# Optimization experiments

Hardware: AMD Instinct MI355X
Metric: run time of the kernel (lower is better)

## Reference

```python
import jax, jax.numpy as jnp
import numpy as np

NUM_HEADS = 16

def setup_inputs() -> dict:
    key = jax.random.key(0)
    ks = jax.random.split(key, 5)
    b, c, w, h = 2, 1024, 48, 48
    sc = 0.02
    return {
        "x": jax.random.normal(ks[0], (b, c, w, h), jnp.float32),
        "Wqkv": jax.random.normal(ks[1], (3 * c, c), jnp.float32) * sc,
        "bqkv": jax.random.normal(ks[2], (3 * c,), jnp.float32) * sc,
        "Wo": jax.random.normal(ks[3], (c, c), jnp.float32) * sc,
        "bo": jax.random.normal(ks[4], (c,), jnp.float32) * sc,
    }

def reference(x, Wqkv, bqkv, Wo, bo):
    b, c, w, h = x.shape
    n = NUM_HEADS
    hd = c // n
    s = w * h
    # [b,c,w,h] -> tokens [b, s, c]
    xs = x.transpose(0, 2, 3, 1).reshape(b, s, c)
    qkv = xs @ Wqkv.T + bqkv                       # [b, s, 3c]
    # rearrange 'b s (three n hd) -> three b n s hd'
    qkv = qkv.reshape(b, s, 3, n, hd).transpose(2, 0, 3, 1, 4)
    q, k, v = qkv[0], qkv[1], qkv[2]               # [b, n, s, hd]
    score = jnp.einsum('bnqh,bnkh->bnqk', q, k) / jnp.sqrt(jnp.float32(hd))
    # module uses a soft causal mask: subtract 10000 above the diagonal
    mask = 10000.0 * jnp.triu(jnp.ones((s, s), dtype=score.dtype), k=1)
    attn = jax.nn.softmax(score - mask, axis=-1)   # [b, n, s, s]
    z = jnp.einsum('bnqk,bnkh->bqnh', attn, v).reshape(b, s, c)
    out = z @ Wo.T + bo                            # [b, s, c]
    return out.reshape(b, w, h, c).transpose(0, 3, 1, 2)
```

## Files before the change

kernel.cpp:

```cpp
#include <hip/hip_runtime.h>

typedef __bf16 bf16;
typedef __bf16 bf16x8 __attribute__((ext_vector_type(8)));
typedef float floatx4 __attribute__((ext_vector_type(4)));

static constexpr int S = 2304;
static constexpr int C = 1024;
static constexpr int NHEAD = 16;
static constexpr int HDIM = 64;
static constexpr int BATCH = 2;
static constexpr float QSCALE = 0.18033688011112042f;
static constexpr int QSPLIT = 12;
static constexpr int NACC = S - QSPLIT * 64;

__global__ __launch_bounds__(256) void k_zero(float4* __restrict__ p, int n4) {
  int i = blockIdx.x * 256 + threadIdx.x;
  if (i < n4) p[i] = float4{0.f, 0.f, 0.f, 0.f};
}

__global__ __launch_bounds__(256) void k_convert2(const float* __restrict__ s1,
                                                  bf16* __restrict__ d1, int n1,
                                                  const float* __restrict__ s2,
                                                  bf16* __restrict__ d2) {
  int i = blockIdx.x * 256 + threadIdx.x;
  const float* s;
  bf16* d;
  int idx;
  if (i < n1) { s = s1; d = d1; idx = i; }
  else        { s = s2; d = d2; idx = i - n1; }
  float4 a = *(const float4*)(s + (size_t)idx * 8);
  float4 b = *(const float4*)(s + (size_t)idx * 8 + 4);
  bf16x8 o;
  o[0] = (bf16)a.x; o[1] = (bf16)a.y; o[2] = (bf16)a.z; o[3] = (bf16)a.w;
  o[4] = (bf16)b.x; o[5] = (bf16)b.y; o[6] = (bf16)b.z; o[7] = (bf16)b.w;
  *(bf16x8*)(d + (size_t)idx * 8) = o;
}

__global__ __launch_bounds__(256) void k_transpose(const float* __restrict__ x,
                                                   bf16* __restrict__ xs) {
  __shared__ bf16 T[64 * 72];
  int c0 = blockIdx.x * 64, t0 = blockIdx.y * 64, b = blockIdx.z;
  int tid = threadIdx.x;
  const float* xb = x + (size_t)b * C * S;
#pragma unroll
  for (int it = 0; it < 4; ++it) {
    int idx = it * 256 + tid;
    int rc = idx >> 4, t4 = idx & 15;
    float4 v = *(const float4*)(xb + (size_t)(c0 + rc) * S + t0 + t4 * 4);
    T[(t4 * 4 + 0) * 72 + rc] = (bf16)v.x;
    T[(t4 * 4 + 1) * 72 + rc] = (bf16)v.y;
    T[(t4 * 4 + 2) * 72 + rc] = (bf16)v.z;
    T[(t4 * 4 + 3) * 72 + rc] = (bf16)v.w;
  }
  __syncthreads();
  bf16* xsb = xs + (size_t)b * S * C;
#pragma unroll
  for (int it = 0; it < 2; ++it) {
    int idx = it * 256 + tid;
    int rt = idx >> 3, c8 = idx & 7;
    bf16x8 v;
#pragma unroll
    for (int i = 0; i < 8; ++i) v[i] = T[rt * 72 + c8 * 8 + i];
    *(bf16x8*)(xsb + (size_t)(t0 + rt) * C + c0 + c8 * 8) = v;
  }
}

__device__ __forceinline__ void g2l16(const bf16* g, bf16* l) {
  __builtin_amdgcn_global_load_lds(
      (const __attribute__((address_space(1))) void*)g,
      (__attribute__((address_space(3))) void*)l, 16, 0, 0);
}

template <int EPI>
__global__ __launch_bounds__(256) void k_gemm_bt(const bf16* __restrict__ A,
                                                 const bf16* __restrict__ Bt,
                                                 const float* __restrict__ bias,
                                                 bf16* __restrict__ q,
                                                 bf16* __restrict__ k,
                                                 bf16* __restrict__ v,
                                                 float* __restrict__ outf) {
  constexpr int K = C;
  __shared__ bf16 As[128 * 64];
  __shared__ bf16 Bs[128 * 64];
  int tid = threadIdx.x;
  int w = tid >> 6, lane = tid & 63, ln = lane & 15, quad = lane >> 4;
  int m0 = blockIdx.y * 128, n0 = blockIdx.x * 128;
  int moff = (w >> 1) * 64, noff = (w & 1) * 64;
  floatx4 acc[4][4] = {};

  int sr[4], sc[4];
#pragma unroll
  for (int it = 0; it < 4; ++it) {
    int L = (it * 4 + w) * 64 + lane;
    sr[it] = L >> 3;
    sc[it] = (L & 7) ^ (sr[it] & 7);
  }

  for (int k0 = 0; k0 < K; k0 += 64) {
    __syncthreads();
#pragma unroll
    for (int it = 0; it < 4; ++it) {
      int cb = (it * 4 + w) * 64;
      g2l16(A + (size_t)(m0 + sr[it]) * K + k0 + sc[it] * 8, As + cb * 8);
      g2l16(Bt + (size_t)(n0 + sr[it]) * K + k0 + sc[it] * 8, Bs + cb * 8);
    }
    __syncthreads();
#pragma unroll
    for (int t = 0; t < 2; ++t) {
      bf16x8 af[4], bfr[4];
#pragma unroll
      for (int i = 0; i < 4; ++i) {
        int ra = moff + i * 16 + ln;
        af[i]  = *(const bf16x8*)(As + ra * 64 + (((t * 4 + quad) ^ (ra & 7))) * 8);
        int rb = noff + i * 16 + ln;
        bfr[i] = *(const bf16x8*)(Bs + rb * 64 + (((t * 4 + quad) ^ (rb & 7))) * 8);
      }
#pragma unroll
      for (int im = 0; im < 4; ++im)
#pragma unroll
        for (int in = 0; in < 4; ++in)
          acc[im][in] = __builtin_amdgcn_mfma_f32_16x16x32_bf16(
              af[im], bfr[in], acc[im][in], 0, 0, 0);
    }
  }

  int bidx = (m0 >= S) ? 1 : 0;
  if (EPI == 0) {
#pragma unroll
    for (int in = 0; in < 4; ++in) {
      int j = n0 + noff + in * 16 + ln;
      float bv = bias[j];
      int three = j >> 10;
      int head = (j >> 6) & 15;
      int hdi = j & 63;
#pragma unroll
      for (int im = 0; im < 4; ++im) {
        int mbase = m0 + moff + im * 16 + quad * 4;
        int tb = mbase - bidx * S;
        if (three == 2) {
          union { ushort4 u; bf16 h[4]; } P;
#pragma unroll
          for (int r = 0; r < 4; ++r) P.h[r] = (bf16)(acc[im][in][r] + bv);
          *(ushort4*)(v + ((size_t)(bidx * NHEAD + head) * HDIM + hdi) * S + tb) = P.u;
        } else if (three == 0) {
          bf16* dst = q + ((size_t)(bidx * NHEAD + head) * S + tb) * HDIM + hdi;
#pragma unroll
          for (int r = 0; r < 4; ++r)
            dst[(size_t)r * HDIM] = (bf16)((acc[im][in][r] + bv) * QSCALE);
        } else {
          bf16* dst = k + ((size_t)(bidx * NHEAD + head) * S + tb) * HDIM + hdi;
#pragma unroll
          for (int r = 0; r < 4; ++r) dst[(size_t)r * HDIM] = (bf16)(acc[im][in][r] + bv);
        }
      }
    }
  } else {
#pragma unroll
    for (int in = 0; in < 4; ++in) {
      int co = n0 + noff + in * 16 + ln;
      float bv = bias[co];
#pragma unroll
      for (int im = 0; im < 4; ++im) {
        int mbase = m0 + moff + im * 16 + quad * 4;
        int tb = mbase - bidx * S;
        float4 st;
        st.x = acc[im][in][0] + bv;
        st.y = acc[im][in][1] + bv;
        st.z = acc[im][in][2] + bv;
        st.w = acc[im][in][3] + bv;
        *(float4*)(outf + ((size_t)bidx * C + co) * S + tb) = st;
      }
    }
  }
}

__global__ __launch_bounds__(256) void k_attn_part(const bf16* __restrict__ Qg,
                                                   const bf16* __restrict__ Kg,
                                                   const bf16* __restrict__ Vtg,
                                                   bf16* __restrict__ z,
                                                   float* __restrict__ Oacc,
                                                   float* __restrict__ Lacc) {
  __shared__ bf16 Ks[2][64 * 64];
  __shared__ bf16 Vs[2][64 * 64];
  __shared__ bf16 Pt[64 * 64];
  int i = blockIdx.x;
  int xcd = i & 7, jj = i >> 3;
  int grp = jj / 72, j = jj % 72;
  int bh = xcd + 8 * grp;
  int qi, lo, hi;
  bool single = false;
  if (j < 36) {
    qi = 35 - j / 3;
    int c = j % 3;
    lo = c * (qi + 1) / 3;
    hi = (c + 1) * (qi + 1) / 3;
  } else if (j < 60) {
    int t = j - 36;
    qi = 23 - (t >> 1);
    int c = t & 1;
    lo = c * (qi + 1) / 2;
    hi = (c + 1) * (qi + 1) / 2;
  } else {
    qi = 71 - j;
    lo = 0;
    hi = qi + 1;
    single = true;
  }
  int b = bh >> 4, h = bh & 15;
  int tid = threadIdx.x;
  int w = tid >> 6, lane = tid & 63, ln = lane & 15, quad = lane >> 4;
  int q0 = qi * 64;
  int qg = q0 + w * 16 + ln;

  const bf16* kb = Kg + (size_t)bh * S * HDIM;
  const bf16* vb = Vtg + (size_t)bh * HDIM * S;

  int s_row = tid >> 3, s_c8 = tid & 7;
  int s_cs = s_c8 ^ (s_row & 7);
  int s_row2 = s_row + 32;
  int s_cs2 = s_c8 ^ (s_row2 & 7);
  size_t kOff1 = (size_t)s_row * HDIM + s_cs * 8;
  size_t kOff2 = (size_t)s_row2 * HDIM + s_cs2 * 8;
  size_t vOff1 = (size_t)s_row * S + s_cs * 8;
  size_t vOff2 = (size_t)s_row2 * S + s_cs2 * 8;

  const bf16* qb = Qg + ((size_t)bh * S + qg) * HDIM + quad * 8;
  bf16x8 qf0 = *(const bf16x8*)qb;
  bf16x8 qf1 = *(const bf16x8*)(qb + 32);

  float lsum = 0.f;
  floatx4 o_acc[4] = {};

  int prow = w * 16 + ln;
  int psw = ln & 7;
  bf16* ptw = Pt + prow * 64 + (quad & 1) * 4;
  const bf16* ptr = Pt + prow * 64;

  const bf16* kb0 = kb + (size_t)lo * 64 * HDIM;
  const bf16* vb0 = vb + (size_t)lo * 64;
  g2l16(kb0 + kOff1, Ks[0] + tid * 8);
  g2l16(vb0 + vOff1, Vs[0] + tid * 8);
  g2l16(kb0 + kOff2, Ks[0] + (256 + tid) * 8);
  g2l16(vb0 + vOff2, Vs[0] + (256 + tid) * 8);

  const bf16* kbn = kb0 + (size_t)64 * HDIM;
  const bf16* vbn = vb0 + 64;

#pragma unroll 1
  for (int kt = lo; kt < hi; ++kt) {
    int cur = (kt - lo) & 1;
    __syncthreads();

    if (kt + 1 < hi) {
      bf16* kd = Ks[1 - cur];
      bf16* vd = Vs[1 - cur];
      g2l16(kbn + kOff1, kd + tid * 8);
      g2l16(vbn + vOff1, vd + tid * 8);
      g2l16(kbn + kOff2, kd + (256 + tid) * 8);
      g2l16(vbn + vOff2, vd + (256 + tid) * 8);
      kbn += (size_t)64 * HDIM;
      vbn += 64;
    }

    floatx4 s_acc[4] = {};
#pragma unroll
    for (int kf = 0; kf < 4; ++kf) {
      int row = kf * 16 + ln;
      int sw = row & 7;
      bf16x8 k0 = *(const bf16x8*)(Ks[cur] + row * 64 + (sw ^ quad) * 8);
      bf16x8 k1 = *(const bf16x8*)(Ks[cur] + row * 64 + ((4 ^ sw) ^ quad) * 8);
      s_acc[kf] = __builtin_amdgcn_mfma_f32_16x16x32_bf16(k0, qf0, s_acc[kf], 0, 0, 0);
      s_acc[kf] = __builtin_amdgcn_mfma_f32_16x16x32_bf16(k1, qf1, s_acc[kf], 0, 0, 0);
    }

    if (kt < qi) {
#pragma unroll
      for (int kf = 0; kf < 4; ++kf) {
        union { ushort4 u; bf16 hh[4]; } P;
#pragma unroll
        for (int rr = 0; rr < 4; ++rr) {
          float pv = exp2f(s_acc[kf][rr]);
          lsum += pv;
          P.hh[rr] = (bf16)pv;
        }
        *(ushort4*)(ptw + (((kf * 2 + (quad >> 1)) ^ psw)) * 8) = P.u;
      }
    } else {
#pragma unroll
      for (int kf = 0; kf < 4; ++kf) {
        union { ushort4 u; bf16 hh[4]; } P;
#pragma unroll
        for (int rr = 0; rr < 4; ++rr) {
          int kl = kf * 16 + quad * 4 + rr;
          float pv = (kl > w * 16 + ln) ? 0.f : exp2f(s_acc[kf][rr]);
          lsum += pv;
          P.hh[rr] = (bf16)pv;
        }
        *(ushort4*)(ptw + (((kf * 2 + (quad >> 1)) ^ psw)) * 8) = P.u;
      }
    }

#pragma unroll
    for (int t = 0; t < 2; ++t) {
      bf16x8 pf = *(const bf16x8*)(ptr + (((t * 4 + quad) ^ psw)) * 8);
#pragma unroll
      for (int hf = 0; hf < 4; ++hf) {
        int row = hf * 16 + ln;
        int sw = row & 7;
        bf16x8 vf = *(const bf16x8*)(Vs[cur] + row * 64 + (((t * 4 + quad) ^ sw)) * 8);
        o_acc[hf] = __builtin_amdgcn_mfma_f32_16x16x32_bf16(vf, pf, o_acc[hf], 0, 0, 0);
      }
    }
  }

  lsum += __shfl_xor(lsum, 16);
  lsum += __shfl_xor(lsum, 32);

  if (single) {
    float inv = 1.f / lsum;
    bf16* dst = z + ((size_t)b * S + qg) * C + h * HDIM + quad * 4;
#pragma unroll
    for (int hf = 0; hf < 4; ++hf) {
      union { ushort4 u; bf16 hh[4]; } P;
#pragma unroll
      for (int rr = 0; rr < 4; ++rr) P.hh[rr] = (bf16)(o_acc[hf][rr] * inv);
      *(ushort4*)(dst + hf * 16) = P.u;
    }
  } else {
    int qa = qg - QSPLIT * 64;
    if (lane < 16) atomicAdd(&Lacc[bh * NACC + qa], lsum);
#pragma unroll
    for (int hf = 0; hf < 4; ++hf)
#pragma unroll
      for (int rr = 0; rr < 4; ++rr)
        atomicAdd(&Oacc[((size_t)bh * 64 + hf * 16 + quad * 4 + rr) * NACC + qa],
                  o_acc[hf][rr]);
  }
}

__global__ __launch_bounds__(256) void k_norm(const float* __restrict__ Oacc,
                                              const float* __restrict__ Lacc,
                                              bf16* __restrict__ z) {
  __shared__ float T[64 * 65];
  int qt = blockIdx.x, bh = blockIdx.y;
  int b = bh >> 4, h = bh & 15;
  int qrel0 = qt * 64;
  int q0 = QSPLIT * 64 + qrel0;
  int tid = threadIdx.x;
  int q4 = (tid & 15) * 4, hd0 = tid >> 4;
  float4 lv = *(const float4*)(Lacc + bh * NACC + qrel0 + q4);
  float inv0 = 1.f / lv.x, inv1 = 1.f / lv.y, inv2 = 1.f / lv.z, inv3 = 1.f / lv.w;
#pragma unroll
  for (int hf = 0; hf < 4; ++hf) {
    int hd = hf * 16 + hd0;
    float4 v = *(const float4*)(Oacc + ((size_t)bh * 64 + hd) * NACC + qrel0 + q4);
    T[(q4 + 0) * 65 + hd] = v.x * inv0;
    T[(q4 + 1) * 65 + hd] = v.y * inv1;
    T[(q4 + 2) * 65 + hd] = v.z * inv2;
    T[(q4 + 3) * 65 + hd] = v.w * inv3;
  }
  __syncthreads();
#pragma unroll
  for (int it = 0; it < 2; ++it) {
    int idx = it * 256 + tid;
    int qq = idx >> 3, c8 = idx & 7;
    bf16x8 o;
#pragma unroll
    for (int k = 0; k < 8; ++k) o[k] = (bf16)T[qq * 65 + c8 * 8 + k];
    *(bf16x8*)(z + ((size_t)b * S + q0 + qq) * C + h * HDIM + c8 * 8) = o;
  }
}

extern "C" void kernel_launch(void* const* d_in, const int* in_sizes, int n_in,
                              void* d_out, int out_size, void* d_ws, size_t ws_size,
                              hipStream_t stream) {
  const float* x    = (const float*)d_in[0];
  const float* Wqkv = (const float*)d_in[1];
  const float* bqkv = (const float*)d_in[2];
  const float* Wo   = (const float*)d_in[3];
  const float* bo   = (const float*)d_in[4];
  float* out = (float*)d_out;

  bf16* ws = (bf16*)d_ws;
  const size_t tok = (size_t)BATCH * S * C;
  bf16* xs   = ws;
  bf16* Qg   = ws + tok;
  bf16* Kg   = ws + 2 * tok;
  bf16* Vtg  = ws + 3 * tok;
  bf16* Wqb  = ws + 4 * tok;
  bf16* Wob  = Wqb + (size_t)3 * C * C;
  float* Oacc = (float*)(Wob + (size_t)C * C);
  float* Lacc = Oacc + (size_t)32 * 64 * NACC;
  bf16* z    = xs;

  k_zero<<<3120, 256, 0, stream>>>((float4*)Oacc, 798720);
  k_convert2<<<2048, 256, 0, stream>>>(Wqkv, Wqb, 3 * C * C / 8, Wo, Wob);
  k_transpose<<<dim3(C / 64, S / 64, BATCH), 256, 0, stream>>>(x, xs);
  k_gemm_bt<0><<<dim3(3 * C / 128, BATCH * S / 128), 256, 0, stream>>>(
      xs, Wqb, bqkv, Qg, Kg, Vtg, nullptr);
  k_attn_part<<<dim3(2304), 256, 0, stream>>>(Qg, Kg, Vtg, z, Oacc, Lacc);
  k_norm<<<dim3(24, 32), 256, 0, stream>>>(Oacc, Lacc, z);
  k_gemm_bt<1><<<dim3(C / 128, BATCH * S / 128), 256, 0, stream>>>(
      z, Wob, bo, nullptr, nullptr, nullptr, out);
}
```

Before: 218.1 us.

## Use 128-query attention tiles with 8 waves sharing K/V and finer key splits

The attention kernel now runs 512-thread blocks that each cover a 128-query tile, so eight waves share every K/V tile loaded into LDS instead of four. Key ranges are split across up to six chunks in a new schedule, and more query rows go through the atomic partial-accumulation path. Waves whose rows lie entirely before the diagonal tile skip the MMA work. The cost is a larger LDS P buffer, wave imbalance near the diagonal, and more atomic traffic and zeroing.

```diff
diff --git a/kernel.cpp b/kernel.cpp
--- a/kernel.cpp
+++ b/kernel.cpp
@@ -10,8 +10,8 @@
 static constexpr int HDIM = 64;
 static constexpr int BATCH = 2;
 static constexpr float QSCALE = 0.18033688011112042f;
-static constexpr int QSPLIT = 12;
-static constexpr int NACC = S - QSPLIT * 64;
+static constexpr int QACC0 = 384;
+static constexpr int NACC = S - QACC0;
 
 __global__ __launch_bounds__(256) void k_zero(float4* __restrict__ p, int n4) {
   int i = blockIdx.x * 256 + threadIdx.x;
@@ -174,7 +174,7 @@
   }
 }
 
-__global__ __launch_bounds__(256) void k_attn_part(const bf16* __restrict__ Qg,
+__global__ __launch_bounds__(512) void k_attn_part(const bf16* __restrict__ Qg,
                                                    const bf16* __restrict__ Kg,
                                                    const bf16* __restrict__ Vtg,
                                                    bf16* __restrict__ z,
@@ -182,47 +182,35 @@
                                                    float* __restrict__ Lacc) {
   __shared__ bf16 Ks[2][64 * 64];
   __shared__ bf16 Vs[2][64 * 64];
-  __shared__ bf16 Pt[64 * 64];
+  __shared__ bf16 Pt[128 * 64];
   int i = blockIdx.x;
   int xcd = i & 7, jj = i >> 3;
-  int grp = jj / 72, j = jj % 72;
+  int grp = jj / 63, j = jj % 63;
   int bh = xcd + 8 * grp;
-  int qi, lo, hi;
-  bool single = false;
-  if (j < 36) {
-    qi = 35 - j / 3;
-    int c = j % 3;
-    lo = c * (qi + 1) / 3;
-    hi = (c + 1) * (qi + 1) / 3;
-  } else if (j < 60) {
-    int t = j - 36;
-    qi = 23 - (t >> 1);
-    int c = t & 1;
-    lo = c * (qi + 1) / 2;
-    hi = (c + 1) * (qi + 1) / 2;
-  } else {
-    qi = 71 - j;
-    lo = 0;
-    hi = qi + 1;
-    single = true;
-  }
+  int qt, c, n;
+  if (j < 18)      { qt = 17 - j / 6;          c = j % 6;  n = 6; }
+  else if (j < 33) { int t = j - 18; qt = 14 - t / 5; c = t % 5; n = 5; }
+  else if (j < 45) { int t = j - 33; qt = 11 - t / 4; c = t % 4; n = 4; }
+  else if (j < 54) { int t = j - 45; qt = 8 - t / 3;  c = t % 3; n = 3; }
+  else if (j < 60) { int t = j - 54; qt = 5 - t / 2;  c = t % 2; n = 2; }
+  else             { qt = 62 - j;              c = 0;      n = 1; }
+  int klen = 2 * qt + 2;
+  int lo = c * klen / n, hi = (c + 1) * klen / n;
+  bool single = (n == 1);
   int b = bh >> 4, h = bh & 15;
   int tid = threadIdx.x;
   int w = tid >> 6, lane = tid & 63, ln = lane & 15, quad = lane >> 4;
-  int q0 = qi * 64;
-  int qg = q0 + w * 16 + ln;
+  int qw = qt * 128 + w * 16;
+  int qg = qw + ln;
+  int dtile = qw >> 6;
 
   const bf16* kb = Kg + (size_t)bh * S * HDIM;
   const bf16* vb = Vtg + (size_t)bh * HDIM * S;
 
   int s_row = tid >> 3, s_c8 = tid & 7;
   int s_cs = s_c8 ^ (s_row & 7);
-  int s_row2 = s_row + 32;
-  int s_cs2 = s_c8 ^ (s_row2 & 7);
-  size_t kOff1 = (size_t)s_row * HDIM + s_cs * 8;
-  size_t kOff2 = (size_t)s_row2 * HDIM + s_cs2 * 8;
-  size_t vOff1 = (size_t)s_row * S + s_cs * 8;
-  size_t vOff2 = (size_t)s_row2 * S + s_cs2 * 8;
+  size_t kOff = (size_t)s_row * HDIM + s_cs * 8;
+  size_t vOff = (size_t)s_row * S + s_cs * 8;
 
   const bf16* qb = Qg + ((size_t)bh * S + qg) * HDIM + quad * 8;
   bf16x8 qf0 = *(const bf16x8*)qb;
@@ -238,10 +226,8 @@
 
   const bf16* kb0 = kb + (size_t)lo * 64 * HDIM;
   const bf16* vb0 = vb + (size_t)lo * 64;
-  g2l16(kb0 + kOff1, Ks[0] + tid * 8);
-  g2l16(vb0 + vOff1, Vs[0] + tid * 8);
-  g2l16(kb0 + kOff2, Ks[0] + (256 + tid) * 8);
-  g2l16(vb0 + vOff2, Vs[0] + (256 + tid) * 8);
+  g2l16(kb0 + kOff, Ks[0] + tid * 8);
+  g2l16(vb0 + vOff, Vs[0] + tid * 8);
 
   const bf16* kbn = kb0 + (size_t)64 * HDIM;
   const bf16* vbn = vb0 + 64;
@@ -252,63 +238,62 @@
     __syncthreads();
 
     if (kt + 1 < hi) {
-      bf16* kd = Ks[1 - cur];
-      bf16* vd = Vs[1 - cur];
-      g2l16(kbn + kOff1, kd + tid * 8);
-      g2l16(vbn + vOff1, vd + tid * 8);
-      g2l16(kbn + kOff2, kd + (256 + tid) * 8);
-      g2l16(vbn + vOff2, vd + (256 + tid) * 8);
+      g2l16(kbn + kOff, Ks[1 - cur] + tid * 8);
+      g2l16(vbn + vOff, Vs[1 - cur] + tid * 8);
       kbn += (size_t)64 * HDIM;
       vbn += 64;
     }
 
-    floatx4 s_acc[4] = {};
-#pragma unroll
-    for (int kf = 0; kf < 4; ++kf) {
-      int row = kf * 16 + ln;
-      int sw = row & 7;
-      bf16x8 k0 = *(const bf16x8*)(Ks[cur] + row * 64 + (sw ^ quad) * 8);
-      bf16x8 k1 = *(const bf16x8*)(Ks[cur] + row * 64 + ((4 ^ sw) ^ quad) * 8);
-      s_acc[kf] = __builtin_amdgcn_mfma_f32_16x16x32_bf16(k0, qf0, s_acc[kf], 0, 0, 0);
-      s_acc[kf] = __builtin_amdgcn_mfma_f32_16x16x32_bf16(k1, qf1, s_acc[kf], 0, 0, 0);
-    }
-
-    if (kt < qi) {
+    if (kt <= dtile) {
+      floatx4 s_acc[4] = {};
 #pragma unroll
       for (int kf = 0; kf < 4; ++kf) {
-        union { ushort4 u; bf16 hh[4]; } P;
-#pragma unroll
-        for (int rr = 0; rr < 4; ++rr) {
-          float pv = exp2f(s_acc[kf][rr]);
-          lsum += pv;
-          P.hh[rr] = (bf16)pv;
+        int row = kf * 16 + ln;
+        int sw = row & 7;
+        bf16x8 k0 = *(const bf16x8*)(Ks[cur] + row * 64 + (sw ^ quad) * 8);
+        bf16x8 k1 = *(const bf16x8*)(Ks[cur] + row * 64 + ((4 ^ sw) ^ quad) * 8);
+        s_acc[kf] = __builtin_amdgcn_mfma_f32_16x16x32_bf16(k0, qf0, s_acc[kf], 0, 0, 0);
+        s_acc[kf] = __builtin_amdgcn_mfma_f32_16x16x32_bf16(k1, qf1, s_acc[kf], 0, 0, 0);
+      }
+
+      if (kt < dtile) {
+#pragma unroll
+        for (int kf = 0; kf < 4; ++kf) {
+          union { ushort4 u; bf16 hh[4]; } P;
+#pragma unroll
+          for (int rr = 0; rr < 4; ++rr) {
+            float pv = exp2f(s_acc[kf][rr]);
+            lsum += pv;
+            P.hh[rr] = (bf16)pv;
+          }
+          *(ushort4*)(ptw + (((kf * 2 + (quad >> 1)) ^ psw)) * 8) = P.u;
         }
-        *(ushort4*)(ptw + (((kf * 2 + (quad >> 1)) ^ psw)) * 8) = P.u;
-      }
-    } else {
-#pragma unroll
-      for (int kf = 0; kf < 4; ++kf) {
-        union { ushort4 u; bf16 hh[4]; } P;
-#pragma unroll
-        for (int rr = 0; rr < 4; ++rr) {
-          int kl = kf * 16 + quad * 4 + rr;
-          float pv = (kl > w * 16 + ln) ? 0.f : exp2f(s_acc[kf][rr]);
-          lsum += pv;
-          P.hh[rr] = (bf16)pv;
+      } else {
+        int qloc = qg - kt * 64;
+#pragma unroll
+        for (int kf = 0; kf < 4; ++kf) {
+          union { ushort4 u; bf16 hh[4]; } P;
+#pragma unroll
+          for (int rr = 0; rr < 4; ++rr) {
+            int kl = kf * 16 + quad * 4 + rr;
+            float pv = (kl > qloc) ? 0.f : exp2f(s_acc[kf][rr]);
+            lsum += pv;
+            P.hh[rr] = (bf16)pv;
+          }
+          *(ushort4*)(ptw + (((kf * 2 + (quad >> 1)) ^ psw)) * 8) = P.u;
         }
-        *(ushort4*)(ptw + (((kf * 2 + (quad >> 1)) ^ psw)) * 8) = P.u;
-      }
-    }
-
-#pragma unroll
-    for (int t = 0; t < 2; ++t) {
-      bf16x8 pf = *(const bf16x8*)(ptr + (((t * 4 + quad) ^ psw)) * 8);
-#pragma unroll
-      for (int hf = 0; hf < 4; ++hf) {
-        int row = hf * 16 + ln;
-        int sw = row & 7;
-        bf16x8 vf = *(const bf16x8*)(Vs[cur] + row * 64 + (((t * 4 + quad) ^ sw)) * 8);
-        o_acc[hf] = __builtin_amdgcn_mfma_f32_16x16x32_bf16(vf, pf, o_acc[hf], 0, 0, 0);
+      }
+
+#pragma unroll
+      for (int t = 0; t < 2; ++t) {
+        bf16x8 pf = *(const bf16x8*)(ptr + (((t * 4 + quad) ^ psw)) * 8);
+#pragma unroll
+        for (int hf = 0; hf < 4; ++hf) {
+          int row = hf * 16 + ln;
+          int sw = row & 7;
+          bf16x8 vf = *(const bf16x8*)(Vs[cur] + row * 64 + (((t * 4 + quad) ^ sw)) * 8);
+          o_acc[hf] = __builtin_amdgcn_mfma_f32_16x16x32_bf16(vf, pf, o_acc[hf], 0, 0, 0);
+        }
       }
     }
   }
@@ -327,7 +312,7 @@
       *(ushort4*)(dst + hf * 16) = P.u;
     }
   } else {
-    int qa = qg - QSPLIT * 64;
+    int qa = qg - QACC0;
     if (lane < 16) atomicAdd(&Lacc[bh * NACC + qa], lsum);
 #pragma unroll
     for (int hf = 0; hf < 4; ++hf)
@@ -345,7 +330,7 @@
   int qt = blockIdx.x, bh = blockIdx.y;
   int b = bh >> 4, h = bh & 15;
   int qrel0 = qt * 64;
-  int q0 = QSPLIT * 64 + qrel0;
+  int q0 = QACC0 + qrel0;
   int tid = threadIdx.x;
   int q4 = (tid & 15) * 4, hd0 = tid >> 4;
   float4 lv = *(const float4*)(Lacc + bh * NACC + qrel0 + q4);
@@ -393,13 +378,13 @@
   float* Lacc = Oacc + (size_t)32 * 64 * NACC;
   bf16* z    = xs;
 
-  k_zero<<<3120, 256, 0, stream>>>((float4*)Oacc, 798720);
+  k_zero<<<3900, 256, 0, stream>>>((float4*)Oacc, 998400);
   k_convert2<<<2048, 256, 0, stream>>>(Wqkv, Wqb, 3 * C * C / 8, Wo, Wob);
   k_transpose<<<dim3(C / 64, S / 64, BATCH), 256, 0, stream>>>(x, xs);
   k_gemm_bt<0><<<dim3(3 * C / 128, BATCH * S / 128), 256, 0, stream>>>(
       xs, Wqb, bqkv, Qg, Kg, Vtg, nullptr);
-  k_attn_part<<<dim3(2304), 256, 0, stream>>>(Qg, Kg, Vtg, z, Oacc, Lacc);
-  k_norm<<<dim3(24, 32), 256, 0, stream>>>(Oacc, Lacc, z);
+  k_attn_part<<<dim3(2016), 512, 0, stream>>>(Qg, Kg, Vtg, z, Oacc, Lacc);
+  k_norm<<<dim3(30, 32), 256, 0, stream>>>(Oacc, Lacc, z);
   k_gemm_bt<1><<<dim3(C / 128, BATCH * S / 128), 256, 0, stream>>>(
       z, Wob, bo, nullptr, nullptr, nullptr, out);
 }
```

Result: slower. 228.5 us (+4.8%).
